# Kernel tuning notes

Hardware: AMD Instinct MI355X
Metric: run time of the kernel (lower is better)

## Reference

```python
import jax, jax.numpy as jnp
import numpy as np

HEADS = 8
DIM_HEAD = 80
BATCH_SIZE = 2  # cfg batch (module init kwarg)


def setup_inputs() -> dict:
    key = jax.random.key(0)
    ks = jax.random.split(key, 6)
    F, S, D = 16, 1024, 640  # frames*batch, latent HW, query_dim
    hidden_states = jax.random.normal(ks[0], (F, S, D), jnp.float32)
    Wq = jax.random.normal(ks[1], (D, D), jnp.float32) * 0.02
    Wk = jax.random.normal(ks[2], (D, D), jnp.float32) * 0.02
    Wv = jax.random.normal(ks[3], (D, D), jnp.float32) * 0.02
    Wo = jax.random.normal(ks[4], (D, D), jnp.float32) * 0.02
    bo = jax.random.normal(ks[5], (D,), jnp.float32) * 0.02
    return {"hidden_states": hidden_states, "Wq": Wq, "Wk": Wk, "Wv": Wv, "Wo": Wo, "bo": bo}


def reference(hidden_states, Wq, Wk, Wv, Wo, bo):
    F, S, D = hidden_states.shape
    h, d = HEADS, DIM_HEAD
    scale = d ** -0.5

    q = hidden_states @ Wq  # [F, S, D]
    k = hidden_states @ Wk
    v = hidden_states @ Wv

    # cross-frame trick: replace every frame's K/V with the FIRST frame of its batch group
    vl = 1 if F < BATCH_SIZE else F // BATCH_SIZE  # video_length
    g = F // vl  # batch groups
    k = jnp.broadcast_to(k.reshape(g, vl, S, D)[:, :1], (g, vl, S, D)).reshape(F, S, D)
    v = jnp.broadcast_to(v.reshape(g, vl, S, D)[:, :1], (g, vl, S, D)).reshape(F, S, D)

    def to_heads(t):  # [F, S, h*d] -> [F*h, S, d]
        return t.reshape(F, S, h, d).transpose(0, 2, 1, 3).reshape(F * h, S, d)

    qh, kh, vh = to_heads(q), to_heads(k), to_heads(v)

    scores = jnp.einsum('bid,bjd->bij', qh, kh) * scale  # [F*h, S, S]
    probs = jax.nn.softmax(scores, axis=-1)
    out = jnp.einsum('bij,bjd->bid', probs, vh)  # [F*h, S, d]

    out = out.reshape(F, h, S, d).transpose(0, 2, 1, 3).reshape(F, S, h * d)
    return out @ Wo + bo
```

## Files before the change

### kernel.cpp

```cpp
#include <hip/hip_runtime.h>
#include <hip/hip_bf16.h>

typedef unsigned short u16;
typedef unsigned int u32;
typedef __attribute__((ext_vector_type(8))) short bf16x8;
typedef __attribute__((ext_vector_type(4))) float f32x4;

#define D640 640

__device__ __forceinline__ float b2f(u16 u) {
  union { u32 i; float f; } x; x.i = ((u32)u) << 16; return x.f;
}
__device__ __forceinline__ u16 f2b(float f) {
  union { __hip_bfloat16 h; u16 u; } c; c.h = __float2bfloat16(f); return c.u;
}
__device__ __forceinline__ u32 pack2(float a, float b) {
  union { __hip_bfloat162 h; u32 u; } c;
  c.h.x = __float2bfloat16(a); c.h.y = __float2bfloat16(b); return c.u;
}
__device__ __forceinline__ bf16x8 pack8(f32x4 lo, f32x4 hi) {
  bf16x8 r;
  r[0] = (short)f2b(lo[0]); r[1] = (short)f2b(lo[1]);
  r[2] = (short)f2b(lo[2]); r[3] = (short)f2b(lo[3]);
  r[4] = (short)f2b(hi[0]); r[5] = (short)f2b(hi[1]);
  r[6] = (short)f2b(hi[2]); r[7] = (short)f2b(hi[3]);
  return r;
}

__global__ void detect_dtype(const u16* __restrict__ hs, u32* __restrict__ flag) {
  __shared__ u32 cnt;
  if (threadIdx.x == 0) cnt = 0;
  __syncthreads();
  int plaus = 0;
#pragma unroll
  for (int i = 0; i < 16; ++i) {
    u16 u = hs[(threadIdx.x * 16 + i) * 2];
    u32 e = (u >> 7) & 0xFF;
    if ((e >= 0x70 && e <= 0x8F) || (u & 0x7FFF) == 0) plaus++;
  }
  atomicAdd(&cnt, (u32)plaus);
  __syncthreads();
  if (threadIdx.x == 0) *flag = (cnt < 2048) ? 1u : 0u;
}

__global__ __launch_bounds__(256) void transpose_w(
    const void* __restrict__ w0, const void* __restrict__ w1,
    const void* __restrict__ w2, const void* __restrict__ w3,
    u16* __restrict__ out, const u32* __restrict__ flag)
{
  __shared__ u16 t[32][33];
  const bool isF32 = (*flag != 0);
  const void* src = blockIdx.z == 0 ? w0 : blockIdx.z == 1 ? w1 : blockIdx.z == 2 ? w2 : w3;
  u16* dst = out + (size_t)blockIdx.z * 409600;
  int tx = threadIdx.x, ty = threadIdx.y;
  int x = blockIdx.x * 32 + tx;
  int y = blockIdx.y * 32 + ty;
  if (isF32) {
    const float* s = (const float*)src;
#pragma unroll
    for (int j = 0; j < 32; j += 8) t[ty + j][tx] = f2b(s[(y + j) * D640 + x]);
  } else {
    const u16* s = (const u16*)src;
#pragma unroll
    for (int j = 0; j < 32; j += 8) t[ty + j][tx] = s[(y + j) * D640 + x];
  }
  __syncthreads();
  int x2 = blockIdx.y * 32 + tx;
  int y2 = blockIdx.x * 32 + ty;
#pragma unroll
  for (int j = 0; j < 32; j += 8) dst[(y2 + j) * D640 + x2] = t[tx][ty + j];
}

__device__ __forceinline__ void gemm_body(
    const void* __restrict__ Av, const u16* __restrict__ BT, void* __restrict__ Cv,
    float scale, const void* __restrict__ bias, bool isF32,
    int aRow0, int aF32mode, int cMode, int bx, int by)
{
  __shared__ __align__(16) u16 Asub[128 * 32];
  __shared__ __align__(16) u16 Bsub[128 * 32];
  const bool aF32 = aF32mode && isF32;
  const bool cF32 = (cMode == 1) && isF32;
  const int tid = threadIdx.x;
  const int lane = tid & 63, w = tid >> 6;
  const int wr = w >> 1, wc = w & 1;
  const int l15 = lane & 15, g = lane >> 4;
  const int rowBase = bx * 128;
  const int colBase = by * 128;

  const int r0 = tid >> 2, r1 = r0 + 64, gc = tid & 3;
  const int ls0 = r0 * 4 + (gc ^ ((r0 >> 1) & 3));
  const int ls1 = r1 * 4 + (gc ^ ((r1 >> 1) & 3));
  const size_t aIdx0 = (size_t)(aRow0 + rowBase + r0) * D640 + gc * 8;
  const size_t aIdx1 = (size_t)(aRow0 + rowBase + r1) * D640 + gc * 8;
  const u16* Bg0 = BT + (colBase + r0) * D640 + gc * 8;
  const u16* Bg1 = BT + (colBase + r1) * D640 + gc * 8;

  int aoff[4], boff[4];
#pragma unroll
  for (int f = 0; f < 4; ++f) {
    int R = wr * 64 + f * 16 + l15;
    aoff[f] = (R * 4 + (g ^ ((R >> 1) & 3))) * 8;
    int Cc = wc * 64 + f * 16 + l15;
    boff[f] = (Cc * 4 + (g ^ ((Cc >> 1) & 3))) * 8;
  }

  f32x4 acc[4][4];
#pragma unroll
  for (int i = 0; i < 4; ++i)
#pragma unroll
    for (int j = 0; j < 4; ++j) acc[i][j] = (f32x4){0.f, 0.f, 0.f, 0.f};

  bf16x8 ra0, ra1, rb0, rb1;
  if (aF32) {
    const float* Af = (const float*)Av;
    ra0 = pack8(*(const f32x4*)(Af + aIdx0), *(const f32x4*)(Af + aIdx0 + 4));
    ra1 = pack8(*(const f32x4*)(Af + aIdx1), *(const f32x4*)(Af + aIdx1 + 4));
  } else {
    const u16* Ab = (const u16*)Av;
    ra0 = *(const bf16x8*)(Ab + aIdx0);
    ra1 = *(const bf16x8*)(Ab + aIdx1);
  }
  rb0 = *(const bf16x8*)Bg0;
  rb1 = *(const bf16x8*)Bg1;

  for (int kt = 0; kt < 20; ++kt) {
    __syncthreads();
    *(bf16x8*)&Asub[ls0 * 8] = ra0;
    *(bf16x8*)&Asub[ls1 * 8] = ra1;
    *(bf16x8*)&Bsub[ls0 * 8] = rb0;
    *(bf16x8*)&Bsub[ls1 * 8] = rb1;
    __syncthreads();
    if (kt < 19) {
      const int k1 = (kt + 1) * 32;
      if (aF32) {
        const float* Af = (const float*)Av;
        ra0 = pack8(*(const f32x4*)(Af + aIdx0 + k1), *(const f32x4*)(Af + aIdx0 + k1 + 4));
        ra1 = pack8(*(const f32x4*)(Af + aIdx1 + k1), *(const f32x4*)(Af + aIdx1 + k1 + 4));
      } else {
        const u16* Ab = (const u16*)Av;
        ra0 = *(const bf16x8*)(Ab + aIdx0 + k1);
        ra1 = *(const bf16x8*)(Ab + aIdx1 + k1);
      }
      rb0 = *(const bf16x8*)(Bg0 + k1);
      rb1 = *(const bf16x8*)(Bg1 + k1);
    }
    bf16x8 a[4], b[4];
#pragma unroll
    for (int f = 0; f < 4; ++f) a[f] = *(const bf16x8*)&Asub[aoff[f]];
#pragma unroll
    for (int f = 0; f < 4; ++f) b[f] = *(const bf16x8*)&Bsub[boff[f]];
    __builtin_amdgcn_s_setprio(1);
#pragma unroll
    for (int i = 0; i < 4; ++i)
#pragma unroll
      for (int j = 0; j < 4; ++j)
        acc[i][j] = __builtin_amdgcn_mfma_f32_16x16x32_bf16(a[i], b[j], acc[i][j], 0, 0, 0);
    __builtin_amdgcn_s_setprio(0);
  }

#pragma unroll
  for (int j = 0; j < 4; ++j) {
    int col = colBase + wc * 64 + j * 16 + l15;
    float bb = 0.f;
    if (bias) bb = cF32 ? ((const float*)bias)[col] : b2f(((const u16*)bias)[col]);
#pragma unroll
    for (int i = 0; i < 4; ++i) {
      int row = rowBase + wr * 64 + i * 16 + g * 4;
#pragma unroll
      for (int r = 0; r < 4; ++r) {
        float v = acc[i][j][r] * scale + bb;
        if (cMode == 2)       ((u16*)Cv)[(size_t)col * 1024 + (row + r)] = f2b(v);
        else if (cF32)        ((float*)Cv)[(size_t)(row + r) * D640 + col] = v;
        else                  ((u16*)Cv)[(size_t)(row + r) * D640 + col] = f2b(v);
      }
    }
  }
}

__global__ __launch_bounds__(256) void gemm_bt(
    const void* __restrict__ Av, const u16* __restrict__ BT, void* __restrict__ Cv,
    float scale, const void* __restrict__ bias, const u32* __restrict__ flag,
    int aRow0, int aF32mode, int cMode)
{
  gemm_body(Av, BT, Cv, scale, bias, (*flag != 0), aRow0, aF32mode, cMode,
            blockIdx.x, blockIdx.y);
}

__global__ __launch_bounds__(256) void gemm_kv(
    const void* __restrict__ hs, const u16* __restrict__ WTk, const u16* __restrict__ WTv,
    u16* __restrict__ Kb, u16* __restrict__ Vb, const u32* __restrict__ flag)
{
  const int z = blockIdx.z;
  const bool isK = (z < 2);
  const int grp = z & 1;
  const u16* bt = isK ? WTk : WTv;
  void* cv = isK ? (void*)(Kb + (size_t)grp * 1024 * 640)
                 : (void*)(Vb + (size_t)grp * 655360);
  gemm_body(hs, bt, cv, 1.f, nullptr, (*flag != 0), grp * 8192, 1, isK ? 0 : 2,
            blockIdx.x, blockIdx.y);
}

__global__ __launch_bounds__(256, 3) void attn_kernel(
    const u16* __restrict__ Q, const u16* __restrict__ K2,
    const u16* __restrict__ VT, u16* __restrict__ AO)
{
  __shared__ __align__(16) u16 Klds[64 * 88 + 8];
  __shared__ __align__(16) u16 Vlds[80 * 64];
  __shared__ __align__(16) u16 Plds[4][32 * 64];

  const int tid = threadIdx.x, lane = tid & 63, w = tid >> 6;
  const int l15 = lane & 15, g = lane >> 4;
  const int kswz = (l15 & 7) << 3;
  const int qc = blockIdx.x, bh = blockIdx.y;
  const int f = bh >> 3, h = bh & 7;
  const int grp = f >> 3;
  u16* Pw = &Plds[w][0];

  const u16* Qp = Q + (size_t)(f * 1024 + qc * 128 + w * 32) * D640 + h * 80;
  const u16* Kp = K2 + (size_t)(grp * 1024) * D640 + h * 80;
  const u16* Vp = VT + (size_t)(grp * 8 + h) * 80 * 1024;

  {
    const bf16x8 z8 = {0, 0, 0, 0, 0, 0, 0, 0};
    if (tid < 64) *(bf16x8*)&Klds[tid * 88 + 80] = z8;
    if (tid == 64) *(bf16x8*)&Klds[64 * 88] = z8;
  }

  bf16x8 qreg[2][3];
#pragma unroll
  for (int qb = 0; qb < 2; ++qb)
#pragma unroll
    for (int dc = 0; dc < 3; ++dc) {
      int dd = dc * 32 + g * 8;
      if (dd < 80) qreg[qb][dc] = *(const bf16x8*)(Qp + (l15 + 16 * qb) * D640 + dd);
      else         qreg[qb][dc] = (bf16x8){0, 0, 0, 0, 0, 0, 0, 0};
    }

  f32x4 acc[2][5];
#pragma unroll
  for (int qb = 0; qb < 2; ++qb)
#pragma unroll
    for (int db = 0; db < 5; ++db) acc[qb][db] = (f32x4){0.f, 0.f, 0.f, 0.f};
  float mreg[2] = {-1e30f, -1e30f};
  float lrow[2] = {0.f, 0.f};

  const u16* gsrc[5];
  u16* ldst[5];
  int step[5];
#pragma unroll
  for (int i = 0; i < 5; ++i) {
    int c = tid + i * 256;
    if (c < 640) {
      int row = c / 10, cc = c - row * 10;
      gsrc[i] = Kp + row * D640 + cc * 8;
      ldst[i] = &Klds[row * 88 + cc * 8];
      step[i] = 64 * D640;
    } else {
      int c2 = c - 640, d = c2 >> 3, cc = c2 & 7;
      gsrc[i] = Vp + d * 1024 + cc * 8;
      ldst[i] = &Vlds[d * 64 + ((cc * 8) ^ ((d & 7) << 3))];
      step[i] = 64;
    }
  }

  bf16x8 pre[5];
#pragma unroll
  for (int i = 0; i < 5; ++i) pre[i] = *(const bf16x8*)gsrc[i];

  for (int it = 0; it < 16; ++it) {
    __syncthreads();
#pragma unroll
    for (int i = 0; i < 5; ++i) *(bf16x8*)ldst[i] = pre[i];
    __syncthreads();
    if (it < 15) {
#pragma unroll
      for (int i = 0; i < 5; ++i) pre[i] = *(const bf16x8*)(gsrc[i] + (it + 1) * step[i]);
    }

    f32x4 st[4][2];
#pragma unroll
    for (int kb = 0; kb < 4; ++kb)
#pragma unroll
      for (int qb = 0; qb < 2; ++qb) st[kb][qb] = (f32x4){0.f, 0.f, 0.f, 0.f};
    __builtin_amdgcn_s_setprio(1);
#pragma unroll
    for (int dc = 0; dc < 3; ++dc)
#pragma unroll
      for (int kb = 0; kb < 4; ++kb) {
        bf16x8 ka = *(const bf16x8*)&Klds[(kb * 16 + l15) * 88 + dc * 32 + g * 8];
        st[kb][0] = __builtin_amdgcn_mfma_f32_16x16x32_bf16(ka, qreg[0][dc], st[kb][0], 0, 0, 0);
        st[kb][1] = __builtin_amdgcn_mfma_f32_16x16x32_bf16(ka, qreg[1][dc], st[kb][1], 0, 0, 0);
      }
    __builtin_amdgcn_s_setprio(0);

    float mt[2];
#pragma unroll
    for (int qb = 0; qb < 2; ++qb) {
      float m01 = fmaxf(fmaxf(st[0][qb][0], st[0][qb][1]), fmaxf(st[0][qb][2], st[0][qb][3]));
      float m23 = fmaxf(fmaxf(st[1][qb][0], st[1][qb][1]), fmaxf(st[1][qb][2], st[1][qb][3]));
      float m45 = fmaxf(fmaxf(st[2][qb][0], st[2][qb][1]), fmaxf(st[2][qb][2], st[2][qb][3]));
      float m67 = fmaxf(fmaxf(st[3][qb][0], st[3][qb][1]), fmaxf(st[3][qb][2], st[3][qb][3]));
      float m = fmaxf(fmaxf(m01, m23), fmaxf(m45, m67));
      m = fmaxf(m, __shfl_xor(m, 16, 64));
      m = fmaxf(m, __shfl_xor(m, 32, 64));
      mt[qb] = m;
    }

    if (__any((mt[0] > mreg[0] + 8.f) || (mt[1] > mreg[1] + 8.f))) {
#pragma unroll
      for (int qb = 0; qb < 2; ++qb) {
        float mn = fmaxf(mreg[qb], mt[qb]);
        float scl = exp2f(mreg[qb] - mn);
        mreg[qb] = mn;
        lrow[qb] *= scl;
        float s_[4];
#pragma unroll
        for (int r = 0; r < 4; ++r)
          s_[r] = __shfl(scl, (lane & 48) | (g * 4 + r), 64);
#pragma unroll
        for (int db = 0; db < 5; ++db)
#pragma unroll
          for (int r = 0; r < 4; ++r) acc[qb][db][r] *= s_[r];
      }
    }

#pragma unroll
    for (int qb = 0; qb < 2; ++qb) {
      float sum = 0.f;
#pragma unroll
      for (int kb = 0; kb < 4; ++kb) {
        float p0 = exp2f(st[kb][qb][0] - mreg[qb]);
        float p1 = exp2f(st[kb][qb][1] - mreg[qb]);
        float p2 = exp2f(st[kb][qb][2] - mreg[qb]);
        float p3 = exp2f(st[kb][qb][3] - mreg[qb]);
        sum += (p0 + p1) + (p2 + p3);
        uint2 pk;
        pk.x = pack2(p0, p1);
        pk.y = pack2(p2, p3);
        *(uint2*)&Pw[(l15 + 16 * qb) * 64 + ((kb * 16 + g * 4) ^ kswz)] = pk;
      }
      sum += __shfl_xor(sum, 16, 64);
      sum += __shfl_xor(sum, 32, 64);
      lrow[qb] += sum;
    }

    __builtin_amdgcn_s_setprio(1);
#pragma unroll
    for (int kc = 0; kc < 2; ++kc) {
      const int ks = (kc * 32 + g * 8) ^ kswz;
      bf16x8 pa0 = *(const bf16x8*)&Pw[l15 * 64 + ks];
      bf16x8 pa1 = *(const bf16x8*)&Pw[(l15 + 16) * 64 + ks];
#pragma unroll
      for (int db = 0; db < 5; ++db) {
        bf16x8 bv = *(const bf16x8*)&Vlds[(db * 16 + l15) * 64 + ks];
        acc[0][db] = __builtin_amdgcn_mfma_f32_16x16x32_bf16(pa0, bv, acc[0][db], 0, 0, 0);
        acc[1][db] = __builtin_amdgcn_mfma_f32_16x16x32_bf16(pa1, bv, acc[1][db], 0, 0, 0);
      }
    }
    __builtin_amdgcn_s_setprio(0);
  }

  u16* Op = AO + (size_t)(f * 1024 + qc * 128 + w * 32) * D640 + h * 80;
#pragma unroll
  for (int qb = 0; qb < 2; ++qb) {
    float i_[4];
#pragma unroll
    for (int r = 0; r < 4; ++r)
      i_[r] = 1.f / __shfl(lrow[qb], (lane & 48) | (g * 4 + r), 64);
#pragma unroll
    for (int db = 0; db < 5; ++db)
#pragma unroll
      for (int r = 0; r < 4; ++r)
        Op[(qb * 16 + g * 4 + r) * D640 + db * 16 + l15] = f2b(acc[qb][db][r] * i_[r]);
  }
}

extern "C" void kernel_launch(void* const* d_in, const int* in_sizes, int n_in,
                              void* d_out, int out_size, void* d_ws, size_t ws_size,
                              hipStream_t stream) {
  (void)in_sizes; (void)n_in; (void)out_size; (void)ws_size;
  const void* hs = d_in[0];
  const void* wq = d_in[1];
  const void* wk = d_in[2];
  const void* wv = d_in[3];
  const void* wo = d_in[4];
  const void* bo = d_in[5];
  u16* ws = (u16*)d_ws;

  u16* WT  = ws;
  u16* Qb  = ws + 1638400;
  u16* Kb  = Qb + 10485760;
  u16* Vb  = Kb + 1310720;
  u16* AOb = Vb + 1310720;
  u32* flag = (u32*)(AOb + 10485760);

  const float QSCALE = 0.11180339887498949f * 1.44269504088896340f;

  detect_dtype<<<1, 256, 0, stream>>>((const u16*)hs, flag);

  transpose_w<<<dim3(20, 20, 4), dim3(32, 8), 0, stream>>>(wq, wk, wv, wo, WT, flag);

  gemm_bt<<<dim3(128, 5), 256, 0, stream>>>(hs, WT, Qb, QSCALE, nullptr, flag, 0, 1, 0);
  gemm_kv<<<dim3(8, 5, 4), 256, 0, stream>>>(hs, WT + 409600, WT + 819200, Kb, Vb, flag);

  attn_kernel<<<dim3(8, 128), 256, 0, stream>>>(Qb, Kb, Vb, AOb);

  gemm_bt<<<dim3(128, 5), 256, 0, stream>>>(AOb, WT + 1228800, d_out, 1.f, bo, flag, 0, 0, 1);
}
```

Measured before the change: 178.1 us.

## Load V fragments directly from global memory instead of staging through LDS

Removes the shared-memory V tile and its cooperative copy. Each wave now loads its V MFMA operands straight from the transposed V buffer in global memory, issued before the softmax exponent work so the latency is hidden. This shrinks LDS use and per-iteration LDS write traffic, which may allow higher occupancy. The cost is that all four waves redundantly fetch the same V data from global/L2 (no sharing), and more registers are used for the bv0/bv1 fragments.

```diff
diff --git a/kernel.cpp b/kernel.cpp
--- a/kernel.cpp
+++ b/kernel.cpp
@@ -205,7 +205,6 @@
     const u16* __restrict__ VT, u16* __restrict__ AO)
 {
   __shared__ __align__(16) u16 Klds[64 * 88 + 8];
-  __shared__ __align__(16) u16 Vlds[80 * 64];
   __shared__ __align__(16) u16 Plds[4][32 * 64];
 
   const int tid = threadIdx.x, lane = tid & 63, w = tid >> 6;
@@ -244,37 +243,33 @@
   float mreg[2] = {-1e30f, -1e30f};
   float lrow[2] = {0.f, 0.f};
 
-  const u16* gsrc[5];
-  u16* ldst[5];
-  int step[5];
-#pragma unroll
-  for (int i = 0; i < 5; ++i) {
+  const bool has3 = (tid < 128);
+  const u16* gsrc[3];
+  u16* ldst[3];
+#pragma unroll
+  for (int i = 0; i < 3; ++i) {
     int c = tid + i * 256;
-    if (c < 640) {
-      int row = c / 10, cc = c - row * 10;
-      gsrc[i] = Kp + row * D640 + cc * 8;
-      ldst[i] = &Klds[row * 88 + cc * 8];
-      step[i] = 64 * D640;
-    } else {
-      int c2 = c - 640, d = c2 >> 3, cc = c2 & 7;
-      gsrc[i] = Vp + d * 1024 + cc * 8;
-      ldst[i] = &Vlds[d * 64 + ((cc * 8) ^ ((d & 7) << 3))];
-      step[i] = 64;
-    }
-  }
-
-  bf16x8 pre[5];
-#pragma unroll
-  for (int i = 0; i < 5; ++i) pre[i] = *(const bf16x8*)gsrc[i];
+    if (c > 639) c = 0;
+    int row = c / 10, cc = c - row * 10;
+    gsrc[i] = Kp + row * D640 + cc * 8;
+    ldst[i] = &Klds[row * 88 + cc * 8];
+  }
+
+  bf16x8 pre0 = *(const bf16x8*)gsrc[0];
+  bf16x8 pre1 = *(const bf16x8*)gsrc[1];
+  bf16x8 pre2 = has3 ? *(const bf16x8*)gsrc[2] : (bf16x8){0,0,0,0,0,0,0,0};
 
   for (int it = 0; it < 16; ++it) {
     __syncthreads();
-#pragma unroll
-    for (int i = 0; i < 5; ++i) *(bf16x8*)ldst[i] = pre[i];
+    *(bf16x8*)ldst[0] = pre0;
+    *(bf16x8*)ldst[1] = pre1;
+    if (has3) *(bf16x8*)ldst[2] = pre2;
     __syncthreads();
     if (it < 15) {
-#pragma unroll
-      for (int i = 0; i < 5; ++i) pre[i] = *(const bf16x8*)(gsrc[i] + (it + 1) * step[i]);
+      const int kstep = (it + 1) * 64 * D640;
+      pre0 = *(const bf16x8*)(gsrc[0] + kstep);
+      pre1 = *(const bf16x8*)(gsrc[1] + kstep);
+      if (has3) pre2 = *(const bf16x8*)(gsrc[2] + kstep);
     }
 
     f32x4 st[4][2];
@@ -323,6 +318,12 @@
           for (int r = 0; r < 4; ++r) acc[qb][db][r] *= s_[r];
       }
     }
+
+    const u16* Vit = Vp + (size_t)l15 * 1024 + it * 64 + g * 8;
+    bf16x8 bv0[5], bv1[5];
+#pragma unroll
+    for (int db = 0; db < 5; ++db)
+      bv0[db] = *(const bf16x8*)(Vit + db * 16 * 1024);
 
 #pragma unroll
     for (int qb = 0; qb < 2; ++qb) {
@@ -344,17 +345,27 @@
       lrow[qb] += sum;
     }
 
+#pragma unroll
+    for (int db = 0; db < 5; ++db)
+      bv1[db] = *(const bf16x8*)(Vit + db * 16 * 1024 + 32);
+
     __builtin_amdgcn_s_setprio(1);
-#pragma unroll
-    for (int kc = 0; kc < 2; ++kc) {
-      const int ks = (kc * 32 + g * 8) ^ kswz;
-      bf16x8 pa0 = *(const bf16x8*)&Pw[l15 * 64 + ks];
-      bf16x8 pa1 = *(const bf16x8*)&Pw[(l15 + 16) * 64 + ks];
+    {
+      const int ks0 = (g * 8) ^ kswz;
+      bf16x8 pa0 = *(const bf16x8*)&Pw[l15 * 64 + ks0];
+      bf16x8 pa1 = *(const bf16x8*)&Pw[(l15 + 16) * 64 + ks0];
 #pragma unroll
       for (int db = 0; db < 5; ++db) {
-        bf16x8 bv = *(const bf16x8*)&Vlds[(db * 16 + l15) * 64 + ks];
-        acc[0][db] = __builtin_amdgcn_mfma_f32_16x16x32_bf16(pa0, bv, acc[0][db], 0, 0, 0);
-        acc[1][db] = __builtin_amdgcn_mfma_f32_16x16x32_bf16(pa1, bv, acc[1][db], 0, 0, 0);
+        acc[0][db] = __builtin_amdgcn_mfma_f32_16x16x32_bf16(pa0, bv0[db], acc[0][db], 0, 0, 0);
+        acc[1][db] = __builtin_amdgcn_mfma_f32_16x16x32_bf16(pa1, bv0[db], acc[1][db], 0, 0, 0);
+      }
+      const int ks1 = (32 + g * 8) ^ kswz;
+      pa0 = *(const bf16x8*)&Pw[l15 * 64 + ks1];
+      pa1 = *(const bf16x8*)&Pw[(l15 + 16) * 64 + ks1];
+#pragma unroll
+      for (int db = 0; db < 5; ++db) {
+        acc[0][db] = __builtin_amdgcn_mfma_f32_16x16x32_bf16(pa0, bv1[db], acc[0][db], 0, 0, 0);
+        acc[1][db] = __builtin_amdgcn_mfma_f32_16x16x32_bf16(pa1, bv1[db], acc[1][db], 0, 0, 0);
       }
     }
     __builtin_amdgcn_s_setprio(0);
```

Measured after the change: 240.5 us. +35.0%, slower.
